# Optimization experiments

Measured on AMD Instinct MI355X. Metric: run time of the kernel, lower is better.

## Reference

```python
import jax, jax.numpy as jnp
import numpy as np

ATTEN_SIZE = 16
HIDDEN = 512


def setup_inputs() -> dict:
    key = jax.random.key(0)
    ks = jax.random.split(key, 6)
    B, S, D_in, H, D_out = 64, 100, 256, HIDDEN, 256
    # xavier-normal-ish scale for weights
    def xav(k, shape):
        fan_in, fan_out = shape
        std = np.sqrt(2.0 / (fan_in + fan_out))
        return jax.random.normal(k, shape, dtype=jnp.float32) * std
    return {
        "x": jax.random.normal(ks[0], (B, S, D_in), dtype=jnp.float32),
        "W0": xav(ks[1], (D_in, H)),
        "b0": jnp.zeros((1, 1, H), dtype=jnp.float32),
        "Wq": xav(ks[2], (H, H)),
        "Wk": xav(ks[3], (H, H)),
        "Wv": xav(ks[4], (H, H)),
        "W1": xav(ks[5], (H, D_out)),
        "b1": jnp.zeros((1, 1, D_out), dtype=jnp.float32),
    }


def reference(x, W0, b0, Wq, Wk, Wv, W1, b1):
    w = ATTEN_SIZE
    win = 2 * w + 1
    B, S = x.shape[0], x.shape[1]
    # pre-attention MLP layer (atten_layer_index = 1)
    h = jax.nn.relu(x @ W0 + b0)  # [B, S, H]
    # sliding-window neighbor gather, matching pad + roll(k) + stack + slice:
    # x_nei[:, i, k_idx] = padded[:, i + 2w - k_idx]  (reversed window order)
    padded = jnp.pad(h, ((0, 0), (w, w), (0, 0)))  # [B, S+2w, H]
    idx = jnp.arange(S)[:, None] + (2 * w - jnp.arange(win))[None, :]
    x_nei = padded[:, idx]
    q = x_nei @ Wq
    k = x_nei @ Wk
    v = x_nei @ Wv
    d = jnp.einsum('bswh,buh_->bswu'.replace('h_', 'sh'[1] + 'h'), q, k) if False else jnp.einsum('bswh,bsuh->bswu', q, k)
    d = d / jnp.sqrt(jnp.float32(HIDDEN))
    alpha = jax.nn.softmax(d, axis=-1)
    wv = jnp.einsum('bswu,bsuh->bswh', alpha, v)
    out = wv.sum(axis=2)  # sum over window rows -> [B, S, H]
    y = jax.nn.relu(out @ W1 + b1)  # [B, S, D_out]
    return y, alpha.reshape(B * S, win, win)
```

## Files before the change

kernel.cpp:

```cpp
#include <hip/hip_runtime.h>

typedef __bf16 bf16x8 __attribute__((ext_vector_type(8)));
typedef float f32x4 __attribute__((ext_vector_type(4)));
typedef unsigned int u32;

__device__ __forceinline__ unsigned short f2bf(float f) {
  unsigned int u = __float_as_uint(f);
  u += 0x7FFFu + ((u >> 16) & 1u);
  return (unsigned short)(u >> 16);
}

__device__ __forceinline__ void gload16(const void* g, void* l) {
  __builtin_amdgcn_global_load_lds(
      (const __attribute__((address_space(1))) u32*)g,
      (__attribute__((address_space(3))) u32*)l, 16, 0, 0);
}

__global__ __launch_bounds__(256) void prep_kernel(
    const float* __restrict__ x, const float* __restrict__ W0,
    const float* __restrict__ Wq, const float* __restrict__ Wk,
    const float* __restrict__ Wv, const float* __restrict__ W1,
    unsigned short* __restrict__ xb, unsigned short* __restrict__ w0t,
    unsigned short* __restrict__ wqkvt, unsigned short* __restrict__ w1t)
{
  __shared__ float tile[32][33];
  const int bid = blockIdx.x, tid = threadIdx.x;
  if (bid < 1600) {
    long i = (long)bid * 1024 + tid * 4;
    float4 v = *(const float4*)(x + i);
    ushort4 o = {f2bf(v.x), f2bf(v.y), f2bf(v.z), f2bf(v.w)};
    *(ushort4*)(xb + i) = o;
    return;
  }
  int id = bid - 1600;
  const float* src; unsigned short* dst;
  int N, DLD, k0, n0, drow0;
  if (id < 128) {
    src = W0; N = 512; dst = w0t; DLD = 256;
    k0 = (id >> 4) * 32; n0 = (id & 15) * 32; drow0 = n0;
  } else if (id < 896) {
    int id1 = id - 128, which = id1 >> 8, rem = id1 & 255;
    src = (which == 0) ? Wq : (which == 1) ? Wk : Wv;
    N = 512; dst = wqkvt; DLD = 512;
    k0 = (rem >> 4) * 32; n0 = (rem & 15) * 32; drow0 = which * 512 + n0;
  } else {
    int id2 = id - 896;
    src = W1; N = 256; dst = w1t; DLD = 512;
    k0 = (id2 >> 3) * 32; n0 = (id2 & 7) * 32; drow0 = n0;
  }
  const int tr = tid >> 5, tc = tid & 31;
#pragma unroll
  for (int rr = 0; rr < 4; ++rr) {
    int kl = tr + rr * 8;
    tile[kl][tc] = src[(long)(k0 + kl) * N + n0 + tc];
  }
  __syncthreads();
#pragma unroll
  for (int rr = 0; rr < 4; ++rr) {
    int nl = tr + rr * 8;
    dst[(long)(drow0 + nl) * DLD + k0 + tc] = f2bf(tile[tc][nl]);
  }
}

template<bool RELU, bool OUT_BF16>
__global__ __launch_bounds__(256) void gemm_tile(
    const unsigned short* __restrict__ A, int lda,
    const unsigned short* __restrict__ Bt, int ldb,
    const float* __restrict__ bias,
    void* __restrict__ Cout, int ldc, int KT)
{
  __shared__ unsigned short As[2][64 * 32];
  __shared__ unsigned short Bs[2][128 * 32];
  const int tid = threadIdx.x;
  const int m0 = blockIdx.x * 64;
  const int n0 = blockIdx.y * 128;
  const int w = tid >> 6, lane = tid & 63;
  const int lr = lane & 15, kq = lane >> 4;
  const int cg  = (tid & 3) ^ ((tid >> 3) & 3);
  const int kqs = kq ^ ((lr >> 1) & 3);

  const unsigned short* Ag  = A  + (long)(m0 + (tid >> 2)) * lda + cg * 8;
  const unsigned short* Bg0 = Bt + (long)(n0 + (tid >> 2)) * ldb + cg * 8;
  const unsigned short* Bg1 = Bg0 + (long)64 * ldb;

  f32x4 acc[4][2];
#pragma unroll
  for (int i = 0; i < 4; i++)
#pragma unroll
    for (int j = 0; j < 2; j++) acc[i][j] = (f32x4){0.f, 0.f, 0.f, 0.f};

#define STAGE(buf, kt) do { int ko = (kt) * 32;                      \
    gload16(Ag + ko,  &As[buf][tid * 8]);                            \
    gload16(Bg0 + ko, &Bs[buf][tid * 8]);                            \
    gload16(Bg1 + ko, &Bs[buf][(tid + 256) * 8]); } while (0)

  STAGE(0, 0);
  __syncthreads();
  int cur = 0;
  for (int kt = 0; kt < KT; ++kt) {
    if (kt + 1 < KT) STAGE(cur ^ 1, kt + 1);
    bf16x8 af[4], bfr[2];
#pragma unroll
    for (int ii = 0; ii < 4; ii++)
      af[ii] = *(const bf16x8*)&As[cur][(16 * ii + lr) * 32 + 8 * kqs];
#pragma unroll
    for (int jj = 0; jj < 2; jj++)
      bfr[jj] = *(const bf16x8*)&Bs[cur][(w * 32 + 16 * jj + lr) * 32 + 8 * kqs];
#pragma unroll
    for (int ii = 0; ii < 4; ii++)
#pragma unroll
      for (int jj = 0; jj < 2; jj++)
        acc[ii][jj] = __builtin_amdgcn_mfma_f32_16x16x32_bf16(af[ii], bfr[jj], acc[ii][jj], 0, 0, 0);
    __syncthreads();
    cur ^= 1;
  }
#undef STAGE

#pragma unroll
  for (int ii = 0; ii < 4; ii++) {
#pragma unroll
    for (int jj = 0; jj < 2; jj++) {
      int col = n0 + w * 32 + 16 * jj + lr;
      float bv = bias ? bias[col] : 0.0f;
#pragma unroll
      for (int r = 0; r < 4; r++) {
        int row = m0 + 16 * ii + 4 * kq + r;
        float v = acc[ii][jj][r] + bv;
        if (RELU) v = fmaxf(v, 0.0f);
        if (OUT_BF16) ((unsigned short*)Cout)[(long)row * ldc + col] = f2bf(v);
        else          ((float*)Cout)[(long)row * ldc + col] = v;
      }
    }
  }
}

__global__ __launch_bounds__(256) void gram_tile(
    const unsigned short* __restrict__ qkv, float* __restrict__ G)
{
  const float scale = 0.044194173824159216f;
  __shared__ unsigned short As[2][64 * 32];
  __shared__ unsigned short Bs[2][64 * 32];
  const int tid = threadIdx.x;
  const int m0 = (blockIdx.x & 1) * 64;
  const int n0 = (blockIdx.x >> 1) * 64;
  const int b  = blockIdx.y;
  const int w = tid >> 6, lane = tid & 63;
  const int lr = lane & 15, kq = lane >> 4;
  const int cg  = (tid & 3) ^ ((tid >> 3) & 3);
  const int kqs = kq ^ ((lr >> 1) & 3);

  const unsigned short* A  = qkv + (long)b * 100 * 1536;
  const unsigned short* Bt = A + 512;
  const unsigned short* Ag = A  + (long)(m0 + (tid >> 2)) * 1536 + cg * 8;
  const unsigned short* Bg = Bt + (long)(n0 + (tid >> 2)) * 1536 + cg * 8;

  f32x4 acc[4];
#pragma unroll
  for (int i = 0; i < 4; i++) acc[i] = (f32x4){0.f, 0.f, 0.f, 0.f};

#define STAGEG(buf, kt) do { int ko = (kt) * 32;                     \
    gload16(Ag + ko, &As[buf][tid * 8]);                             \
    gload16(Bg + ko, &Bs[buf][tid * 8]); } while (0)

  STAGEG(0, 0);
  __syncthreads();
  int cur = 0;
  for (int kt = 0; kt < 16; ++kt) {
    if (kt + 1 < 16) STAGEG(cur ^ 1, kt + 1);
    bf16x8 bk = *(const bf16x8*)&Bs[cur][(16 * w + lr) * 32 + 8 * kqs];
    bf16x8 af[4];
#pragma unroll
    for (int ii = 0; ii < 4; ii++)
      af[ii] = *(const bf16x8*)&As[cur][(16 * ii + lr) * 32 + 8 * kqs];
#pragma unroll
    for (int ii = 0; ii < 4; ii++)
      acc[ii] = __builtin_amdgcn_mfma_f32_16x16x32_bf16(af[ii], bk, acc[ii], 0, 0, 0);
    __syncthreads();
    cur ^= 1;
  }
#undef STAGEG

  float* Gb = G + (long)b * 10000;
  int j = n0 + w * 16 + lr;
#pragma unroll
  for (int ii = 0; ii < 4; ii++) {
#pragma unroll
    for (int r = 0; r < 4; r++) {
      int i = m0 + 16 * ii + 4 * kq + r;
      if (i < 100 && j < 100) Gb[i * 100 + j] = acc[ii][r] * scale;
    }
  }
}

__global__ __launch_bounds__(256) void attn_kernel4(
    const float* __restrict__ G,
    const unsigned short* __restrict__ qkv,
    float* __restrict__ alpha_out,
    unsigned short* __restrict__ outb)
{
  const int blk = blockIdx.x;
  const int b = blk / 25, s0 = (blk % 25) * 4;
  __shared__ float E[4][33][36];
  __shared__ float rinv[4][33];
  __shared__ float beta[4][36];
  const int tid = threadIdx.x;
  const float* Gb = G + (long)b * 10000;

  for (int t = tid; t < 4356; t += 256) {
    int si = t / 1089, r = t - si * 1089;
    int dw = r / 33, du = r - dw * 33;
    int s = s0 + si;
    int i = s + 16 - dw, j = s + 16 - du;
    float v = 0.f;
    if ((unsigned)i < 100u && (unsigned)j < 100u) v = Gb[i * 100 + j];
    E[si][dw][du] = __expf(v);
  }
  __syncthreads();

  for (int t = tid; t < 528; t += 256) {
    int q = t >> 2, g = t & 3;
    int si = q / 33, row = q - si * 33;
    float ssum = 0.f;
    for (int u = g; u < 33; u += 4) ssum += E[si][row][u];
    ssum += __shfl_xor(ssum, 1);
    ssum += __shfl_xor(ssum, 2);
    if (g == 0) rinv[si][row] = 1.0f / ssum;
  }
  __syncthreads();

  for (int t = tid; t < 4356; t += 256) {
    int si = t / 1089, r = t - si * 1089;
    int dw = r / 33;
    alpha_out[(long)(b * 100 + s0 + si) * 1089 + r] = E[si][dw][r - dw * 33] * rinv[si][dw];
  }
  for (int t = tid; t < 528; t += 256) {
    int q = t >> 2, g = t & 3;
    int si = q / 33, col = q - si * 33;
    float sum = 0.f;
    for (int w = g; w < 33; w += 4) sum += E[si][w][col] * rinv[si][w];
    sum += __shfl_xor(sum, 1);
    sum += __shfl_xor(sum, 2);
    if (g == 0) beta[si][col] = sum;
  }
  __syncthreads();

  const unsigned short* vbase = qkv + (long)(b * 100) * 1536 + 1024;
  float a0[4] = {0.f, 0.f, 0.f, 0.f}, a1[4] = {0.f, 0.f, 0.f, 0.f};
  for (int p = s0 - 16; p < s0 + 20; ++p) {
    if ((unsigned)p < 100u) {
      u32 pv = *(const u32*)(vbase + (long)p * 1536 + 2 * tid);
      float v0 = __uint_as_float(pv << 16);
      float v1 = __uint_as_float(pv & 0xFFFF0000u);
#pragma unroll
      for (int si = 0; si < 4; ++si) {
        int u = s0 + si + 16 - p;
        if ((unsigned)u < 33u) {
          float bw = beta[si][u];
          a0[si] = fmaf(bw, v0, a0[si]);
          a1[si] = fmaf(bw, v1, a1[si]);
        }
      }
    }
  }
#pragma unroll
  for (int si = 0; si < 4; ++si) {
    u32 packed = (u32)f2bf(a0[si]) | ((u32)f2bf(a1[si]) << 16);
    *(u32*)(outb + (long)(b * 100 + s0 + si) * 512 + 2 * tid) = packed;
  }
}

extern "C" void kernel_launch(void* const* d_in, const int* in_sizes, int n_in,
                              void* d_out, int out_size, void* d_ws, size_t ws_size,
                              hipStream_t stream) {
  const float* x  = (const float*)d_in[0];
  const float* W0 = (const float*)d_in[1];
  const float* b0 = (const float*)d_in[2];
  const float* Wq = (const float*)d_in[3];
  const float* Wk = (const float*)d_in[4];
  const float* Wv = (const float*)d_in[5];
  const float* W1 = (const float*)d_in[6];
  const float* b1 = (const float*)d_in[7];

  char* ws = (char*)d_ws;
  unsigned short* xb    = (unsigned short*)(ws + 0);
  unsigned short* w0t   = (unsigned short*)(ws + 3276800);
  unsigned short* wqkvt = (unsigned short*)(ws + 3538944);
  unsigned short* w1t   = (unsigned short*)(ws + 5111808);
  unsigned short* h     = (unsigned short*)(ws + 5373952);
  unsigned short* qkv   = (unsigned short*)(ws + 11927552);
  float*          G     = (float*)(ws + 31686656);
  unsigned short* outb  = (unsigned short*)(ws + 34246656);

  float* y_out     = (float*)d_out;
  float* alpha_out = y_out + 6400 * 256;

  prep_kernel<<<2624, 256, 0, stream>>>(x, W0, Wq, Wk, Wv, W1, xb, w0t, wqkvt, w1t);
  gemm_tile<true,  true ><<<dim3(100, 4),  256, 0, stream>>>(xb, 256, w0t, 256, b0, h, 512, 8);
  gemm_tile<false, true ><<<dim3(100, 12), 256, 0, stream>>>(h, 512, wqkvt, 512, nullptr, qkv, 1536, 16);
  gram_tile<<<dim3(4, 64), 256, 0, stream>>>(qkv, G);
  attn_kernel4<<<1600, 256, 0, stream>>>(G, qkv, alpha_out, outb);
  gemm_tile<true,  false><<<dim3(100, 2),  256, 0, stream>>>(outb, 512, w1t, 512, b1, y_out, 256, 16);
}
```

Baseline: 172.8 us.

## Fuse Gram-matrix computation into the sliding-window attention kernel

Replaces the separate Gram kernel and attention kernel with one kernel. Each attention block computes, with MFMA, the 36x36 window of q·kᵀ it needs for its 4 positions and keeps it in shared memory as exponentials. Row sums are then built with a sliding-window update instead of a full reduction per position. This removes one launch and the global write and re-read of the full Gram matrix. In exchange the matrix-multiply work is repeated across overlapping windows, and out-of-range rows are loaded from neighbouring workspace memory, then masked.

```diff
diff --git a/kernel.cpp b/kernel.cpp
--- a/kernel.cpp
+++ b/kernel.cpp
@@ -134,39 +134,43 @@
   }
 }
 
-__global__ __launch_bounds__(256) void gram_tile(
-    const unsigned short* __restrict__ qkv, float* __restrict__ G)
+__global__ __launch_bounds__(256) void fused_gram_attn(
+    const unsigned short* __restrict__ qkv,
+    float* __restrict__ alpha_out,
+    unsigned short* __restrict__ outb)
 {
   const float scale = 0.044194173824159216f;
   __shared__ unsigned short As[2][64 * 32];
   __shared__ unsigned short Bs[2][64 * 32];
+  __shared__ float Ep[36][37];
+  __shared__ float rinvP[4][36];
+  __shared__ float beta[4][36];
+
   const int tid = threadIdx.x;
-  const int m0 = (blockIdx.x & 1) * 64;
-  const int n0 = (blockIdx.x >> 1) * 64;
-  const int b  = blockIdx.y;
+  const int blk = blockIdx.x;
+  const int b = blk / 25, s0 = (blk % 25) * 4;
+  const int i0 = s0 - 16;
   const int w = tid >> 6, lane = tid & 63;
   const int lr = lane & 15, kq = lane >> 4;
   const int cg  = (tid & 3) ^ ((tid >> 3) & 3);
   const int kqs = kq ^ ((lr >> 1) & 3);
 
-  const unsigned short* A  = qkv + (long)b * 100 * 1536;
-  const unsigned short* Bt = A + 512;
-  const unsigned short* Ag = A  + (long)(m0 + (tid >> 2)) * 1536 + cg * 8;
-  const unsigned short* Bg = Bt + (long)(n0 + (tid >> 2)) * 1536 + cg * 8;
+  const unsigned short* Ag =
+      qkv + (long)(b * 100 + i0 + (tid >> 2)) * 1536 + cg * 8;
 
   f32x4 acc[4];
 #pragma unroll
   for (int i = 0; i < 4; i++) acc[i] = (f32x4){0.f, 0.f, 0.f, 0.f};
 
-#define STAGEG(buf, kt) do { int ko = (kt) * 32;                     \
-    gload16(Ag + ko, &As[buf][tid * 8]);                             \
-    gload16(Bg + ko, &Bs[buf][tid * 8]); } while (0)
-
-  STAGEG(0, 0);
+#define STAGEF(buf, kt) do { int ko = (kt) * 32;                     \
+    gload16(Ag + ko,       &As[buf][tid * 8]);                       \
+    gload16(Ag + 512 + ko, &Bs[buf][tid * 8]); } while (0)
+
+  STAGEF(0, 0);
   __syncthreads();
   int cur = 0;
   for (int kt = 0; kt < 16; ++kt) {
-    if (kt + 1 < 16) STAGEG(cur ^ 1, kt + 1);
+    if (kt + 1 < 16) STAGEF(cur ^ 1, kt + 1);
     bf16x8 bk = *(const bf16x8*)&Bs[cur][(16 * w + lr) * 32 + 8 * kqs];
     bf16x8 af[4];
 #pragma unroll
@@ -178,69 +182,55 @@
     __syncthreads();
     cur ^= 1;
   }
-#undef STAGEG
-
-  float* Gb = G + (long)b * 10000;
-  int j = n0 + w * 16 + lr;
-#pragma unroll
-  for (int ii = 0; ii < 4; ii++) {
-#pragma unroll
-    for (int r = 0; r < 4; r++) {
-      int i = m0 + 16 * ii + 4 * kq + r;
-      if (i < 100 && j < 100) Gb[i * 100 + j] = acc[ii][r] * scale;
-    }
-  }
-}
-
-__global__ __launch_bounds__(256) void attn_kernel4(
-    const float* __restrict__ G,
-    const unsigned short* __restrict__ qkv,
-    float* __restrict__ alpha_out,
-    unsigned short* __restrict__ outb)
-{
-  const int blk = blockIdx.x;
-  const int b = blk / 25, s0 = (blk % 25) * 4;
-  __shared__ float E[4][33][36];
-  __shared__ float rinv[4][33];
-  __shared__ float beta[4][36];
-  const int tid = threadIdx.x;
-  const float* Gb = G + (long)b * 10000;
+#undef STAGEF
+
+  {
+    int jl = w * 16 + lr;
+    if (jl < 36) {
+      bool jok = (unsigned)(i0 + jl) < 100u;
+#pragma unroll
+      for (int ii = 0; ii < 3; ii++) {
+#pragma unroll
+        for (int r = 0; r < 4; r++) {
+          int il = 16 * ii + 4 * kq + r;
+          if (il < 36) {
+            bool iok = (unsigned)(i0 + il) < 100u;
+            Ep[il][jl] = (iok && jok) ? __expf(scale * acc[ii][r]) : 1.0f;
+          }
+        }
+      }
+    }
+  }
+  __syncthreads();
+
+  if (tid < 36) {
+    float Wk = 0.f;
+    for (int c = 0; c < 33; ++c) Wk += Ep[tid][c];
+    rinvP[0][tid] = 1.0f / Wk;
+#pragma unroll
+    for (int si = 1; si < 4; ++si) {
+      Wk += Ep[tid][si + 32] - Ep[tid][si - 1];
+      rinvP[si][tid] = 1.0f / Wk;
+    }
+  }
+  __syncthreads();
 
   for (int t = tid; t < 4356; t += 256) {
-    int si = t / 1089, r = t - si * 1089;
-    int dw = r / 33, du = r - dw * 33;
-    int s = s0 + si;
-    int i = s + 16 - dw, j = s + 16 - du;
-    float v = 0.f;
-    if ((unsigned)i < 100u && (unsigned)j < 100u) v = Gb[i * 100 + j];
-    E[si][dw][du] = __expf(v);
-  }
-  __syncthreads();
-
+    int si = t / 1089, rem = t - si * 1089;
+    int dw = rem / 33, du = rem - dw * 33;
+    float a = Ep[si + 32 - dw][si + 32 - du] * rinvP[si][si + 32 - dw];
+    alpha_out[(long)(b * 100 + s0 + si) * 1089 + rem] = a;
+  }
   for (int t = tid; t < 528; t += 256) {
     int q = t >> 2, g = t & 3;
-    int si = q / 33, row = q - si * 33;
-    float ssum = 0.f;
-    for (int u = g; u < 33; u += 4) ssum += E[si][row][u];
-    ssum += __shfl_xor(ssum, 1);
-    ssum += __shfl_xor(ssum, 2);
-    if (g == 0) rinv[si][row] = 1.0f / ssum;
-  }
-  __syncthreads();
-
-  for (int t = tid; t < 4356; t += 256) {
-    int si = t / 1089, r = t - si * 1089;
-    int dw = r / 33;
-    alpha_out[(long)(b * 100 + s0 + si) * 1089 + r] = E[si][dw][r - dw * 33] * rinv[si][dw];
-  }
-  for (int t = tid; t < 528; t += 256) {
-    int q = t >> 2, g = t & 3;
-    int si = q / 33, col = q - si * 33;
+    int si = q / 33, du = q - si * 33;
+    int c = si + 32 - du;
     float sum = 0.f;
-    for (int w = g; w < 33; w += 4) sum += E[si][w][col] * rinv[si][w];
+    for (int r = si + g; r <= si + 32; r += 4)
+      sum += Ep[r][c] * rinvP[si][r];
     sum += __shfl_xor(sum, 1);
     sum += __shfl_xor(sum, 2);
-    if (g == 0) beta[si][col] = sum;
+    if (g == 0) beta[si][du] = sum;
   }
   __syncthreads();
 
@@ -288,8 +278,7 @@
   unsigned short* w1t   = (unsigned short*)(ws + 5111808);
   unsigned short* h     = (unsigned short*)(ws + 5373952);
   unsigned short* qkv   = (unsigned short*)(ws + 11927552);
-  float*          G     = (float*)(ws + 31686656);
-  unsigned short* outb  = (unsigned short*)(ws + 34246656);
+  unsigned short* outb  = (unsigned short*)(ws + 31686656);
 
   float* y_out     = (float*)d_out;
   float* alpha_out = y_out + 6400 * 256;
@@ -297,7 +286,6 @@
   prep_kernel<<<2624, 256, 0, stream>>>(x, W0, Wq, Wk, Wv, W1, xb, w0t, wqkvt, w1t);
   gemm_tile<true,  true ><<<dim3(100, 4),  256, 0, stream>>>(xb, 256, w0t, 256, b0, h, 512, 8);
   gemm_tile<false, true ><<<dim3(100, 12), 256, 0, stream>>>(h, 512, wqkvt, 512, nullptr, qkv, 1536, 16);
-  gram_tile<<<dim3(4, 64), 256, 0, stream>>>(qkv, G);
-  attn_kernel4<<<1600, 256, 0, stream>>>(G, qkv, alpha_out, outb);
+  fused_gram_attn<<<1600, 256, 0, stream>>>(qkv, alpha_out, outb);
   gemm_tile<true,  false><<<dim3(100, 2),  256, 0, stream>>>(outb, 512, w1t, 512, b1, y_out, 256, 16);
 }
```

After: 172.2 us. No clear change (-0.3%).
